# Kernel tuning notes

Measured on AMD Instinct MI355X. Metric: run time of the kernel, lower is better.

Reference implementation:

```python
import jax, jax.numpy as jnp
import numpy as np

B, S = 16, 512
VD, TD, H, NH = 768, 768, 1024, 16
HD = H // NH
MAXREL = 128
THRESH = 2.0 / 3.0


def _bitlinear(x, W, b):
    # BitNet b1.58 eval-mode: ternary-quantize weights, rescale, dense matmul
    s = jnp.clip(jnp.mean(jnp.abs(W)), 1e-5, 1000.0)
    wn = jnp.clip(W / s, -10.0, 10.0)
    q = jnp.where(wn > THRESH, 1.0, jnp.where(wn < -THRESH, -1.0, 0.0))
    return x @ (q * s).T + b


def _ln(x, g, b, eps=1e-5):
    m = jnp.mean(x, axis=-1, keepdims=True)
    v = jnp.mean((x - m) ** 2, axis=-1, keepdims=True)
    return (x - m) * jax.lax.rsqrt(v + eps) * g + b


def setup_inputs() -> dict:
    key = jax.random.key(0)
    ks = jax.random.split(key, 10)
    def n(k, shape, std=0.02):
        return jax.random.normal(k, shape, dtype=jnp.float32) * std
    return dict(
        vision_features=jax.random.normal(ks[0], (B, VD), dtype=jnp.float32),
        text_features=jax.random.normal(ks[1], (B, S, TD), dtype=jnp.float32),
        W_vp=n(ks[2], (H, VD)), b_vp=jnp.zeros((H,), jnp.float32),
        W_tp=n(ks[3], (H, TD)), b_tp=jnp.zeros((H,), jnp.float32),
        W_tqkv=n(ks[4], (3 * H, H)), b_tqkv=jnp.zeros((3 * H,), jnp.float32),
        W_vout=n(ks[5], (H, H)), b_vout=jnp.zeros((H,), jnp.float32),
        W_tout=n(ks[6], (H, H)), b_tout=jnp.zeros((H,), jnp.float32),
        g_tn=jnp.ones((H,), jnp.float32), be_tn=jnp.zeros((H,), jnp.float32),
        g_i2t=jnp.ones((H,), jnp.float32), be_i2t=jnp.zeros((H,), jnp.float32),
        g_t2i=jnp.ones((H,), jnp.float32), be_t2i=jnp.zeros((H,), jnp.float32),
        alpha_i2t=jnp.zeros((1,), jnp.float32),
        alpha_t2i=jnp.zeros((1,), jnp.float32),
        rel_embed=n(ks[7], (2 * MAXREL + 1, NH)),
        text_mask=jnp.ones((B, S), dtype=bool),
    )


def reference(vision_features, text_features, W_vp, b_vp, W_tp, b_tp,
              W_tqkv, b_tqkv, W_vout, b_vout, W_tout, b_tout,
              g_tn, be_tn, g_i2t, be_i2t, g_t2i, be_t2i,
              alpha_i2t, alpha_t2i, rel_embed, text_mask):
    scale = HD ** -0.5
    vision_proj = _bitlinear(vision_features, W_vp, b_vp)            # [B,H]
    text_proj = _bitlinear(text_features, W_tp, b_tp)                # [B,S,H]

    # --- text self-attention with relative-position bias ---
    qkv = _bitlinear(_ln(text_proj, g_tn, be_tn), W_tqkv, b_tqkv)    # [B,S,3H]
    qkv = qkv.reshape(B, S, 3, NH, HD).transpose(2, 0, 3, 1, 4)      # [3,B,nh,S,hd]
    q, k, v = qkv[0], qkv[1], qkv[2]
    attn = jnp.einsum('bhqd,bhkd->bhqk', q, k) * scale
    coords = jnp.arange(S)
    rel = jnp.clip(coords[:, None] - coords[None, :], -MAXREL, MAXREL) + MAXREL
    attn = attn + rel_embed[rel].transpose(2, 0, 1)[None]            # +[1,nh,S,S]
    attn = jnp.where(text_mask[:, None, None, :], attn, -1e9)
    attn = jax.nn.softmax(attn, axis=-1)
    text_self = jnp.einsum('bhqk,bhkd->bhqd', attn, v)
    text_self = text_self.transpose(0, 2, 1, 3).reshape(B, S, H)
    text_self = text_proj + text_self                                # residual

    # --- image -> text cross-attention (vision token queries text) ---
    vq = jnp.broadcast_to(vision_proj[:, None], (B, S, H))
    vq = vq.reshape(B, S, NH, HD).transpose(0, 2, 1, 3)              # [B,nh,S,hd]
    tkv = text_self.reshape(B, S, NH, HD).transpose(0, 2, 1, 3)      # [B,nh,S,hd]
    i2t = jnp.einsum('bhqd,bhkd->bhqk', vq, tkv) * scale
    i2t = jnp.where(text_mask[:, None, None, :], i2t, -1e9)
    i2t = jax.nn.softmax(i2t, axis=-1)
    i2t_out = jnp.einsum('bhqk,bhkd->bhqd', i2t, tkv)
    i2t_out = i2t_out.transpose(0, 2, 1, 3).reshape(B, S, H).mean(axis=1)
    i2t_out = _ln(i2t_out, g_i2t, be_i2t)                            # [B,H]
    fused_vision = vision_proj + alpha_i2t * _bitlinear(i2t_out, W_vout, b_vout)

    # --- text -> image cross-attention (text queries single vision token) ---
    tq = text_self.reshape(B, S, NH, HD).transpose(0, 2, 1, 3)       # [B,nh,S,hd]
    vkv = vision_proj.reshape(B, 1, NH, HD).transpose(0, 2, 1, 3)    # [B,nh,1,hd]
    t2i = jnp.einsum('bhqd,bhkd->bhqk', tq, vkv) * scale             # [B,nh,S,1]
    t2i = jax.nn.softmax(t2i, axis=-1)
    t2i_out = jnp.einsum('bhqk,bhkd->bhqd', t2i, vkv)
    t2i_out = t2i_out.transpose(0, 2, 1, 3).reshape(B, S, H)
    t2i_out = _ln(t2i_out, g_t2i, be_t2i)
    fused_text = text_self + alpha_t2i * _bitlinear(t2i_out, W_tout, b_tout)

    return fused_vision, fused_text
```

## Files before the change

### kernel.cpp

```cpp
#include <hip/hip_runtime.h>
#include <cstdint>

#define B_   16
#define S_   512
#define VD_  768
#define TD_  768
#define H_   1024
#define NH_  16
#define HD_  64
#define H3_  3072

typedef __attribute__((ext_vector_type(8))) short bf16x8;
typedef __attribute__((ext_vector_type(4))) float f32x4;

__device__ __forceinline__ float b2f(unsigned short h) {
  union { unsigned u; float f; } x; x.u = ((unsigned)h) << 16; return x.f;
}
__device__ __forceinline__ unsigned short f2b(float f) {
  union { float f; unsigned u; } x; x.f = f;
  unsigned r = x.u + 0x7fffu + ((x.u >> 16) & 1u);
  return (unsigned short)(r >> 16);
}
__device__ __forceinline__ unsigned cvt_pk_bf16(float lo, float hi) {
  unsigned r;
  __asm__("v_cvt_pk_bf16_f32 %0, %1, %2" : "=v"(r) : "v"(lo), "v"(hi));
  return r;
}
__device__ __forceinline__ float fexp2(float x) {
#if __has_builtin(__builtin_amdgcn_exp2f)
  return __builtin_amdgcn_exp2f(x);
#else
  return exp2f(x);
#endif
}

__device__ __forceinline__ void gload_lds16(const void* g, void* lds) {
  __builtin_amdgcn_global_load_lds(
      (const __attribute__((address_space(1))) unsigned int*)g,
      (__attribute__((address_space(3))) unsigned int*)lds, 16, 0, 0);
}
__device__ __forceinline__ void lds_wave_fence() {
  __asm__ __volatile__("s_waitcnt lgkmcnt(0)" ::: "memory");
}

__global__ __launch_bounds__(256) void k_abssum_cvt(const float* __restrict__ w0, int n0,
                                                    const float* __restrict__ w1, int n1,
                                                    const float* __restrict__ w2, int n2,
                                                    const float* __restrict__ w3, int n3,
                                                    const float* __restrict__ w4, int n4,
                                                    double* __restrict__ partials,
                                                    const float* __restrict__ cvt_in,
                                                    unsigned short* __restrict__ cvt_out,
                                                    int cvt_n4) {
  int y = blockIdx.y;
  if (y == 5) {
    for (int i = blockIdx.x * 256 + threadIdx.x; i < cvt_n4; i += 128 * 256) {
      float4 v = ((const float4*)cvt_in)[i];
      ushort4 o; o.x = f2b(v.x); o.y = f2b(v.y); o.z = f2b(v.z); o.w = f2b(v.w);
      ((ushort4*)cvt_out)[i] = o;
    }
    return;
  }
  const float* w = y == 0 ? w0 : y == 1 ? w1 : y == 2 ? w2 : y == 3 ? w3 : w4;
  int n4q = (y == 0 ? n0 : y == 1 ? n1 : y == 2 ? n2 : y == 3 ? n3 : n4) >> 2;
  double s = 0.0;
  for (int i = blockIdx.x * 256 + threadIdx.x; i < n4q; i += 128 * 256) {
    float4 v = ((const float4*)w)[i];
    s += (double)fabsf(v.x) + (double)fabsf(v.y) + (double)fabsf(v.z) + (double)fabsf(v.w);
  }
#pragma unroll
  for (int off = 32; off > 0; off >>= 1) s += __shfl_down(s, off, 64);
  __shared__ double red[4];
  if ((threadIdx.x & 63) == 0) red[threadIdx.x >> 6] = s;
  __syncthreads();
  if (threadIdx.x == 0)
    partials[y * 128 + blockIdx.x] = red[0] + red[1] + red[2] + red[3];
}

__global__ __launch_bounds__(512) void k_sumfin(const double* __restrict__ partials,
                                                double* __restrict__ sums) {
  int wave = threadIdx.x >> 6, lane = threadIdx.x & 63;
  if (wave >= 5) return;
  double s = partials[wave * 128 + lane] + partials[wave * 128 + 64 + lane];
#pragma unroll
  for (int off = 32; off > 0; off >>= 1) s += __shfl_down(s, off, 64);
  if (lane == 0) sums[wave] = s;
}

__global__ __launch_bounds__(256) void k_quant5(const float* __restrict__ w0, int n0,
                                                const float* __restrict__ w1, int n1,
                                                const float* __restrict__ w2, int n2,
                                                const float* __restrict__ w3, int n3,
                                                const float* __restrict__ w4, int n4,
                                                unsigned short* __restrict__ q0,
                                                unsigned short* __restrict__ q1,
                                                unsigned short* __restrict__ q2,
                                                unsigned short* __restrict__ q3,
                                                unsigned short* __restrict__ q4,
                                                const double* __restrict__ sum,
                                                float* __restrict__ s_out) {
  int y = blockIdx.y;
  const float* w = y == 0 ? w0 : y == 1 ? w1 : y == 2 ? w2 : y == 3 ? w3 : w4;
  unsigned short* q = y == 0 ? q0 : y == 1 ? q1 : y == 2 ? q2 : y == 3 ? q3 : q4;
  int n = y == 0 ? n0 : y == 1 ? n1 : y == 2 ? n2 : y == 3 ? n3 : n4;
  double s = fmin(fmax(sum[y] / (double)n, 1e-5), 1000.0);
  if (blockIdx.x == 0 && threadIdx.x == 0) s_out[y] = (float)s;
  int i = blockIdx.x * 256 + threadIdx.x;
  if (i < n) {
    double wn = (double)w[i] / s;
    unsigned short o = 0;
    if (wn > (2.0 / 3.0)) o = 0x3F80u;
    else if (wn < -(2.0 / 3.0)) o = 0xBF80u;
    q[i] = o;
  }
}

__global__ __launch_bounds__(256) void k_rowmat(const float* __restrict__ A,
                                                const unsigned short* __restrict__ W,
                                                const float* __restrict__ sptr,
                                                const float* __restrict__ bias,
                                                float* __restrict__ Cf,
                                                unsigned short* __restrict__ Cb,
                                                const float* __restrict__ resid,
                                                const float* __restrict__ alpha,
                                                int N, int K) {
  const int t = threadIdx.x, lane = t & 63;
  const int w_idx = blockIdx.x * 4 + (t >> 6);
  const int m = w_idx / N, n = w_idx - m * N;
  const int Kper = K >> 6;
  const float* a = A + (size_t)m * K + lane * Kper;
  const unsigned short* w = W + (size_t)n * K + lane * Kper;
  float acc = 0.f;
  for (int k = 0; k < Kper; k += 4) {
    float4 av = *(const float4*)(a + k);
    ushort4 wv = *(const ushort4*)(w + k);
    acc += av.x * b2f(wv.x) + av.y * b2f(wv.y) + av.z * b2f(wv.z) + av.w * b2f(wv.w);
  }
#pragma unroll
  for (int off = 32; off > 0; off >>= 1) acc += __shfl_down(acc, off, 64);
  if (lane == 0) {
    float v = acc * sptr[0] + bias[n];
    if (resid) v = resid[w_idx] + alpha[0] * v;
    Cf[w_idx] = v;
    if (Cb) Cb[w_idx] = f2b(v);
  }
}

__global__ __launch_bounds__(256) void k_ln(const float* __restrict__ x,
                                            const float* __restrict__ g,
                                            const float* __restrict__ be,
                                            float* __restrict__ of,
                                            unsigned short* __restrict__ ob) {
  int row = blockIdx.x, t = threadIdx.x;
  const float4* xr = (const float4*)(x + (size_t)row * H_);
  float4 v = xr[t];
  float s = v.x + v.y + v.z + v.w;
  float s2 = v.x * v.x + v.y * v.y + v.z * v.z + v.w * v.w;
#pragma unroll
  for (int off = 32; off > 0; off >>= 1) { s += __shfl_down(s, off, 64); s2 += __shfl_down(s2, off, 64); }
  __shared__ float rs[4], rs2[4];
  if ((t & 63) == 0) { rs[t >> 6] = s; rs2[t >> 6] = s2; }
  __syncthreads();
  s = rs[0] + rs[1] + rs[2] + rs[3];
  s2 = rs2[0] + rs2[1] + rs2[2] + rs2[3];
  float mean = s * (1.0f / H_);
  float var = s2 * (1.0f / H_) - mean * mean;
  float rstd = rsqrtf(var + 1e-5f);
  const float4 gv = ((const float4*)g)[t];
  const float4 bv = ((const float4*)be)[t];
  float4 o;
  o.x = (v.x - mean) * rstd * gv.x + bv.x;
  o.y = (v.y - mean) * rstd * gv.y + bv.y;
  o.z = (v.z - mean) * rstd * gv.z + bv.z;
  o.w = (v.w - mean) * rstd * gv.w + bv.w;
  if (of) ((float4*)(of + (size_t)row * H_))[t] = o;
  if (ob) {
    ushort4 ou; ou.x = f2b(o.x); ou.y = f2b(o.y); ou.z = f2b(o.z); ou.w = f2b(o.w);
    ((ushort4*)(ob + (size_t)row * H_))[t] = ou;
  }
}

template <int OUTB, int VT>
__global__ __launch_bounds__(512) void k_gemm(const unsigned short* __restrict__ A,
                                              const unsigned short* __restrict__ W,
                                              const float* __restrict__ sptr,
                                              const float* __restrict__ bias,
                                              float* __restrict__ Cf,
                                              unsigned short* __restrict__ Cb,
                                              unsigned short* __restrict__ vt,
                                              int M, int N, int K) {
  __shared__ __align__(16) unsigned short As[3][128 * 64];
  __shared__ __align__(16) unsigned short Bs[3][256 * 64];
  const int t = threadIdx.x, wave = t >> 6, lane = t & 63, quad = lane >> 4, l16 = lane & 15;
  const int bm = blockIdx.y * 128, bn = blockIdx.x * 256;
  const int wm = (wave >> 2) * 64, wn = (wave & 3) * 64;
  f32x4 acc[4][4];
#pragma unroll
  for (int i = 0; i < 4; ++i)
#pragma unroll
    for (int j = 0; j < 4; ++j) acc[i][j] = f32x4{0.f, 0.f, 0.f, 0.f};

  const int srow = lane >> 3;
  const int kcg = (lane & 7) ^ srow;
  auto stage = [&](int kt, int buf) {
    const int k0 = kt * 64;
#pragma unroll
    for (int c = 0; c < 2; ++c) {
      int row = c * 64 + wave * 8 + srow;
      gload_lds16(A + (size_t)(bm + row) * K + k0 + kcg * 8,
                  &As[buf][(c * 64 + wave * 8) * 64]);
    }
#pragma unroll
    for (int c = 0; c < 4; ++c) {
      int row = c * 64 + wave * 8 + srow;
      gload_lds16(W + (size_t)(bn + row) * K + k0 + kcg * 8,
                  &Bs[buf][(c * 64 + wave * 8) * 64]);
    }
  };

  const int NT = K >> 6;
  stage(0, 0);
  stage(1, 1);
  for (int kt = 0; kt < NT; ++kt) {
    if (kt + 1 < NT) __asm__ __volatile__("s_waitcnt vmcnt(6)" ::: "memory");
    else             __asm__ __volatile__("s_waitcnt vmcnt(0)" ::: "memory");
    __asm__ __volatile__("s_barrier" ::: "memory");
    if (kt + 2 < NT) stage(kt + 2, (kt + 2) % 3);
    const unsigned short* Ab = &As[kt % 3][0];
    const unsigned short* Bb = &Bs[kt % 3][0];
#pragma unroll
    for (int ks = 0; ks < 2; ++ks) {
      bf16x8 af[4], bfr[4];
#pragma unroll
      for (int i = 0; i < 4; ++i) {
        int R = wm + i * 16 + l16;
        af[i] = *(const bf16x8*)&Ab[R * 64 + (((ks * 4 + quad) ^ (R & 7)) * 8)];
      }
#pragma unroll
      for (int j = 0; j < 4; ++j) {
        int R = wn + j * 16 + l16;
        bfr[j] = *(const bf16x8*)&Bb[R * 64 + (((ks * 4 + quad) ^ (R & 7)) * 8)];
      }
      __builtin_amdgcn_s_setprio(1);
#pragma unroll
      for (int i = 0; i < 4; ++i)
#pragma unroll
        for (int j = 0; j < 4; ++j)
          acc[i][j] = __builtin_amdgcn_mfma_f32_16x16x32_bf16(af[i], bfr[j], acc[i][j], 0, 0, 0);
      __builtin_amdgcn_s_setprio(0);
    }
  }
  float s = sptr[0];

  if (VT && bn >= 2 * H_) {
    __syncthreads();
    unsigned short* T = &As[0][0] + wave * 1152;
    const int h = (bn + wn - 2 * H_) >> 6;
    const int b = (bm + wm) >> 9, s0 = (bm + wm) & (S_ - 1);
    const int chunk0 = lane * 2;
#pragma unroll
    for (int j = 0; j < 4; ++j) {
      int n = bn + wn + j * 16 + l16;
      float bv = bias[n];
#pragma unroll
      for (int i = 0; i < 4; ++i)
#pragma unroll
        for (int r = 0; r < 4; ++r)
          T[l16 * 72 + i * 16 + quad * 4 + r] = f2b(acc[i][j][r] * s + bv);
      lds_wave_fence();
#pragma unroll
      for (int cc = 0; cc < 2; ++cc) {
        int ch = chunk0 + cc, dr = ch >> 3, k8 = ch & 7;
        uint4 val = *(const uint4*)&T[dr * 72 + k8 * 8];
        *(uint4*)(vt + ((size_t)(b * NH_ + h) * HD_ + j * 16 + dr) * S_ + s0 + k8 * 8) = val;
      }
      lds_wave_fence();
    }
    return;
  }

#pragma unroll
  for (int j = 0; j < 4; ++j) {
    int n = bn + wn + j * 16 + l16;
    float bv = bias[n];
#pragma unroll
    for (int i = 0; i < 4; ++i) {
#pragma unroll
      for (int r = 0; r < 4; ++r) {
        int m = bm + wm + i * 16 + quad * 4 + r;
        float v = acc[i][j][r] * s + bv;
        if (OUTB) Cb[(size_t)m * N + n] = f2b(v);
        else      Cf[(size_t)m * N + n] = v;
      }
    }
  }
}

__global__ __launch_bounds__(256) void k_flash(const unsigned short* __restrict__ qkv,
                                               const unsigned short* __restrict__ vt,
                                               const float* __restrict__ tp,
                                               const float* __restrict__ rel,
                                               const float* __restrict__ trow,
                                               const float* __restrict__ a_t2i,
                                               float* __restrict__ out_text,
                                               unsigned short* __restrict__ ts_b) {
  const int qt = blockIdx.x, h = blockIdx.y, b = blockIdx.z;
  __shared__ __align__(16) unsigned short Qs[64 * 64];
  __shared__ __align__(16) unsigned short Ks[2][64 * 64];
  __shared__ __align__(16) unsigned short Vs[2][64 * 64];
  __shared__ __align__(16) unsigned short Ps[4][16 * 72];
  __shared__ float rels[257];
  const int t = threadIdx.x, wave = t >> 6, lane = t & 63, quad = lane >> 4, l16 = lane & 15;
  const int srow = lane >> 3;
  const int kcg = (lane & 7) ^ srow;
  const float LOG2E = 1.4426950408889634f;
  const float SC = 0.125f * LOG2E;

  for (int i = t; i < 257; i += 256) rels[i] = rel[i * NH_ + h] * LOG2E;

  auto stage_kv = [&](int kt, int buf) {
#pragma unroll
    for (int c = 0; c < 2; ++c) {
      int row = (wave * 2 + c) * 8 + srow;
      gload_lds16(qkv + (size_t)(b * S_ + kt * 64 + row) * H3_ + H_ + h * HD_ + kcg * 8,
                  &Ks[buf][(wave * 2 + c) * 512]);
      gload_lds16(vt + ((size_t)(b * NH_ + h) * HD_ + row) * S_ + kt * 64 + kcg * 8,
                  &Vs[buf][(wave * 2 + c) * 512]);
    }
  };

#pragma unroll
  for (int c = 0; c < 2; ++c) {
    int row = (wave * 2 + c) * 8 + srow;
    gload_lds16(qkv + (size_t)(b * S_ + qt * 64 + row) * H3_ + h * HD_ + kcg * 8,
                &Qs[(wave * 2 + c) * 512]);
  }
  stage_kv(0, 0);

  float mrun = -1e30f, lrun = 0.f;
  f32x4 o[4];
#pragma unroll
  for (int j = 0; j < 4; ++j) o[j] = f32x4{0.f, 0.f, 0.f, 0.f};

  bf16x8 aq0, aq1;
  bool qloaded = false;
  const int qg = qt * 64 + wave * 16 + l16;

  for (int kt = 0; kt < 8; ++kt) {
    const int cur = kt & 1;
    __syncthreads();
    if (kt < 7) stage_kv(kt + 1, cur ^ 1);

    if (!qloaded) {
      int R = wave * 16 + l16;
      aq0 = *(const bf16x8*)&Qs[R * 64 + ((quad ^ (R & 7)) * 8)];
      aq1 = *(const bf16x8*)&Qs[R * 64 + (((4 + quad) ^ (R & 7)) * 8)];
      qloaded = true;
    }

    const int dq = qt - kt;
    const bool uni = (dq >= 3) || (dq <= -3);
    const float bu = uni ? rels[dq >= 3 ? 256 : 0] : 0.f;

    float pv[4][4];
#pragma unroll
    for (int j = 0; j < 4; ++j) {
      int R = j * 16 + l16;
      bf16x8 kb0 = *(const bf16x8*)&Ks[cur][R * 64 + ((quad ^ (R & 7)) * 8)];
      bf16x8 kb1 = *(const bf16x8*)&Ks[cur][R * 64 + (((4 + quad) ^ (R & 7)) * 8)];
      f32x4 z = f32x4{0.f, 0.f, 0.f, 0.f};
      z = __builtin_amdgcn_mfma_f32_16x16x32_bf16(kb0, aq0, z, 0, 0, 0);
      z = __builtin_amdgcn_mfma_f32_16x16x32_bf16(kb1, aq1, z, 0, 0, 0);
      if (uni) {
#pragma unroll
        for (int r = 0; r < 4; ++r) pv[j][r] = z[r] * SC + bu;
      } else {
        const int kg0 = kt * 64 + j * 16 + quad * 4;
#pragma unroll
        for (int r = 0; r < 4; ++r) {
          int rix = min(max(qg - kg0 - r, -128), 128) + 128;
          pv[j][r] = z[r] * SC + rels[rix];
        }
      }
    }
    float x = pv[0][0];
#pragma unroll
    for (int j = 0; j < 4; ++j)
#pragma unroll
      for (int r = 0; r < 4; ++r) x = fmaxf(x, pv[j][r]);
    x = fmaxf(x, __shfl_xor(x, 16, 64));
    x = fmaxf(x, __shfl_xor(x, 32, 64));
    if (!__all(x <= mrun)) {
      float mn = fmaxf(mrun, x);
      float al = fexp2(mrun - mn);
      mrun = mn;
      lrun *= al;
      float al0 = __shfl(al, quad * 4 + 0, 64);
      float al1 = __shfl(al, quad * 4 + 1, 64);
      float al2 = __shfl(al, quad * 4 + 2, 64);
      float al3 = __shfl(al, quad * 4 + 3, 64);
#pragma unroll
      for (int jd = 0; jd < 4; ++jd) {
        o[jd][0] *= al0; o[jd][1] *= al1; o[jd][2] *= al2; o[jd][3] *= al3;
      }
    }
    float rsum = 0.f;
#pragma unroll
    for (int j = 0; j < 4; ++j)
#pragma unroll
      for (int r = 0; r < 4; ++r) {
        float p = fexp2(pv[j][r] - mrun);
        pv[j][r] = p;
        rsum += p;
      }
    rsum += __shfl_xor(rsum, 16, 64);
    rsum += __shfl_xor(rsum, 32, 64);
    lrun += rsum;
    unsigned char* psb = (unsigned char*)&Ps[wave][0] + l16 * 144 + quad * 8;
#pragma unroll
    for (int j = 0; j < 4; ++j) {
      uint2 pk;
      pk.x = cvt_pk_bf16(pv[j][0], pv[j][1]);
      pk.y = cvt_pk_bf16(pv[j][2], pv[j][3]);
      *(uint2*)(psb + j * 32) = pk;
    }
    lds_wave_fence();
#pragma unroll
    for (int ks = 0; ks < 2; ++ks) {
      bf16x8 ap = *(const bf16x8*)&Ps[wave][l16 * 72 + ks * 32 + quad * 8];
#pragma unroll
      for (int jd = 0; jd < 4; ++jd) {
        int R = jd * 16 + l16;
        int C = ks * 4 + quad;
        bf16x8 vb = *(const bf16x8*)&Vs[cur][R * 64 + ((C ^ (R & 7)) * 8)];
        o[jd] = __builtin_amdgcn_mfma_f32_16x16x32_bf16(ap, vb, o[jd], 0, 0, 0);
      }
    }
  }
  float a2 = a_t2i[0];
  float il[4];
#pragma unroll
  for (int r = 0; r < 4; ++r) {
    float lr = __shfl(lrun, quad * 4 + r, 64);
    il[r] = 1.0f / lr;
  }
#pragma unroll
  for (int jd = 0; jd < 4; ++jd) {
#pragma unroll
    for (int r = 0; r < 4; ++r) {
      int g = b * S_ + qt * 64 + wave * 16 + quad * 4 + r;
      int col = h * HD_ + jd * 16 + l16;
      float ov = o[jd][r] * il[r];
      float ts = tp[(size_t)g * H_ + col] + ov;
      ts_b[(size_t)g * H_ + col] = f2b(ts);
      out_text[(size_t)g * H_ + col] = ts + a2 * trow[b * H_ + col];
    }
  }
}

__global__ __launch_bounds__(256) void k_i2t(const unsigned short* __restrict__ vp_b,
                                             const unsigned short* __restrict__ ts_b,
                                             float* __restrict__ i2t_out) {
  const int h = blockIdx.x & 15, b = blockIdx.x >> 4;
  __shared__ float sc[512];
  __shared__ float red[4];
  __shared__ float qv[64];
  __shared__ float ored[4][64];
  const int t = threadIdx.x;
  if (t < 64) qv[t] = b2f(vp_b[b * H_ + h * HD_ + t]);
  __syncthreads();
  for (int k = t; k < 512; k += 256) {
    const unsigned short* kr = ts_b + (size_t)(b * S_ + k) * H_ + h * HD_;
    float acc = 0.f;
#pragma unroll
    for (int dc = 0; dc < 8; ++dc) {
      uint4 u = *(const uint4*)(kr + dc * 8);
      const unsigned short* p = (const unsigned short*)&u;
#pragma unroll
      for (int i = 0; i < 8; ++i) acc += qv[dc * 8 + i] * b2f(p[i]);
    }
    sc[k] = acc * 0.125f;
  }
  __syncthreads();
  float m = -1e30f;
  for (int k = t; k < 512; k += 256) m = fmaxf(m, sc[k]);
#pragma unroll
  for (int off = 1; off < 64; off <<= 1) m = fmaxf(m, __shfl_xor(m, off, 64));
  if ((t & 63) == 0) red[t >> 6] = m;
  __syncthreads();
  m = fmaxf(fmaxf(red[0], red[1]), fmaxf(red[2], red[3]));
  __syncthreads();
  float ls = 0.f;
  for (int k = t; k < 512; k += 256) { float p = __expf(sc[k] - m); sc[k] = p; ls += p; }
#pragma unroll
  for (int off = 1; off < 64; off <<= 1) ls += __shfl_xor(ls, off, 64);
  if ((t & 63) == 0) red[t >> 6] = ls;
  __syncthreads();
  float tot = red[0] + red[1] + red[2] + red[3];
  const int d = t & 63, grp = t >> 6;
  float acc = 0.f;
  for (int k = grp; k < 512; k += 4)
    acc += sc[k] * b2f(ts_b[(size_t)(b * S_ + k) * H_ + h * HD_ + d]);
  ored[grp][d] = acc;
  __syncthreads();
  if (t < 64)
    i2t_out[b * H_ + h * HD_ + t] = (ored[0][t] + ored[1][t] + ored[2][t] + ored[3][t]) / tot;
}

extern "C" void kernel_launch(void* const* d_in, const int* in_sizes, int n_in,
                              void* d_out, int out_size, void* d_ws, size_t ws_size,
                              hipStream_t stream) {
  const float* vf     = (const float*)d_in[0];
  const float* tf     = (const float*)d_in[1];
  const float* W_vp   = (const float*)d_in[2];
  const float* b_vp   = (const float*)d_in[3];
  const float* W_tp   = (const float*)d_in[4];
  const float* b_tp   = (const float*)d_in[5];
  const float* W_tqkv = (const float*)d_in[6];
  const float* b_tqkv = (const float*)d_in[7];
  const float* W_vout = (const float*)d_in[8];
  const float* b_vout = (const float*)d_in[9];
  const float* W_tout = (const float*)d_in[10];
  const float* b_tout = (const float*)d_in[11];
  const float* g_tn   = (const float*)d_in[12];
  const float* be_tn  = (const float*)d_in[13];
  const float* g_i2t  = (const float*)d_in[14];
  const float* be_i2t = (const float*)d_in[15];
  const float* g_t2i  = (const float*)d_in[16];
  const float* be_t2i = (const float*)d_in[17];
  const float* a_i2t  = (const float*)d_in[18];
  const float* a_t2i  = (const float*)d_in[19];
  const float* rel    = (const float*)d_in[20];

  size_t off = 0;
  auto alloc = [&](size_t bytes) -> void* {
    void* p = (char*)d_ws + off;
    off += (bytes + 255) & ~(size_t)255;
    return p;
  };
  double* sums     = (double*)alloc(64);
  double* partials = (double*)alloc(5 * 128 * 8);
  float* scales    = (float*)alloc(64);
  unsigned short* q_vp   = (unsigned short*)alloc((size_t)H_ * VD_ * 2);
  unsigned short* q_tp   = (unsigned short*)alloc((size_t)H_ * TD_ * 2);
  unsigned short* q_tqkv = (unsigned short*)alloc((size_t)H3_ * H_ * 2);
  unsigned short* q_vout = (unsigned short*)alloc((size_t)H_ * H_ * 2);
  unsigned short* q_tout = (unsigned short*)alloc((size_t)H_ * H_ * 2);
  unsigned short* tf_b   = (unsigned short*)alloc((size_t)B_ * S_ * TD_ * 2);
  float* text_proj       = (float*)alloc((size_t)B_ * S_ * H_ * 4);
  unsigned short* ln_tp  = (unsigned short*)alloc((size_t)B_ * S_ * H_ * 2);
  unsigned short* qkv    = (unsigned short*)alloc((size_t)B_ * S_ * H3_ * 2);
  unsigned short* vt     = (unsigned short*)alloc((size_t)B_ * NH_ * HD_ * S_ * 2);
  unsigned short* ts_b   = (unsigned short*)alloc((size_t)B_ * S_ * H_ * 2);
  float* vision_proj     = (float*)alloc((size_t)B_ * H_ * 4);
  unsigned short* vp_b   = (unsigned short*)alloc((size_t)B_ * H_ * 2);
  float* ln_t2i_f        = (float*)alloc((size_t)B_ * H_ * 4);
  float* trow            = (float*)alloc((size_t)B_ * H_ * 4);
  float* i2t_out         = (float*)alloc((size_t)B_ * H_ * 4);
  float* ln_i2t_f        = (float*)alloc((size_t)B_ * H_ * 4);

  float* out_vision = (float*)d_out;
  float* out_text   = (float*)d_out + B_ * H_;

  k_abssum_cvt<<<dim3(128, 6), 256, 0, stream>>>(W_vp, H_ * VD_, W_tp, H_ * TD_,
                                                 W_tqkv, H3_ * H_, W_vout, H_ * H_,
                                                 W_tout, H_ * H_, partials,
                                                 tf, tf_b, B_ * S_ * TD_ / 4);
  k_sumfin<<<1, 512, 0, stream>>>(partials, sums);
  k_quant5<<<dim3((H3_ * H_ + 255) / 256, 5), 256, 0, stream>>>(
      W_vp, H_ * VD_, W_tp, H_ * TD_, W_tqkv, H3_ * H_, W_vout, H_ * H_, W_tout, H_ * H_,
      q_vp, q_tp, q_tqkv, q_vout, q_tout, sums, scales);

  k_rowmat<<<(B_ * H_) / 4, 256, 0, stream>>>(vf, q_vp, scales + 0, b_vp,
                                              vision_proj, vp_b, nullptr, nullptr, H_, VD_);
  k_ln<<<B_, 256, 0, stream>>>(vision_proj, g_t2i, be_t2i, ln_t2i_f, nullptr);
  k_rowmat<<<(B_ * H_) / 4, 256, 0, stream>>>(ln_t2i_f, q_tout, scales + 4, b_tout,
                                              trow, nullptr, nullptr, nullptr, H_, H_);

  k_gemm<0, 0><<<dim3(H_ / 256, (B_ * S_) / 128), 512, 0, stream>>>(
      tf_b, q_tp, scales + 1, b_tp, text_proj, nullptr, nullptr, B_ * S_, H_, TD_);
  k_ln<<<B_ * S_, 256, 0, stream>>>(text_proj, g_tn, be_tn, nullptr, ln_tp);
  k_gemm<1, 1><<<dim3(H3_ / 256, (B_ * S_) / 128), 512, 0, stream>>>(
      ln_tp, q_tqkv, scales + 2, b_tqkv, nullptr, qkv, vt, B_ * S_, H3_, H_);
  k_flash<<<dim3(S_ / 64, NH_, B_), 256, 0, stream>>>(qkv, vt, text_proj, rel, trow, a_t2i,
                                                      out_text, ts_b);
  k_i2t<<<B_ * NH_, 256, 0, stream>>>(vp_b, ts_b, i2t_out);
  k_ln<<<B_, 256, 0, stream>>>(i2t_out, g_i2t, be_i2t, ln_i2t_f, nullptr);
  k_rowmat<<<(B_ * H_) / 4, 256, 0, stream>>>(ln_i2t_f, q_vout, scales + 3, b_vout,
                                              out_vision, nullptr, vision_proj, a_i2t, H_, H_);
}
```

Measured before the change: 397.0 us.

## Rewrite projection GEMMs as 256-row tiles with ping-pong interleaved prefetch

Replaces the 128x256 triple-buffered GEMM with a 256xNF*64 tile kernel using double-buffered LDS and an 8-wave schedule. Each k-step is split into four quarter phases, with global-to-LDS prefetches spread between barriers and MFMA blocks at raised priority. Tile shapes change to 256x128 for the text projection and 256x192 for the QKV GEMM, giving grids of 8x32 and 16x32 blocks. The goal is better overlap of loads with MFMA and better wave occupancy across CUs. The cost is many more barriers per k-step and a larger per-wave accumulator footprint.

```diff
diff --git a/kernel.cpp b/kernel.cpp
--- a/kernel.cpp
+++ b/kernel.cpp
@@ -180,117 +180,177 @@
   }
 }
 
-template <int OUTB, int VT>
-__global__ __launch_bounds__(512) void k_gemm(const unsigned short* __restrict__ A,
-                                              const unsigned short* __restrict__ W,
-                                              const float* __restrict__ sptr,
-                                              const float* __restrict__ bias,
-                                              float* __restrict__ Cf,
-                                              unsigned short* __restrict__ Cb,
-                                              unsigned short* __restrict__ vt,
-                                              int M, int N, int K) {
-  __shared__ __align__(16) unsigned short As[3][128 * 64];
-  __shared__ __align__(16) unsigned short Bs[3][256 * 64];
-  const int t = threadIdx.x, wave = t >> 6, lane = t & 63, quad = lane >> 4, l16 = lane & 15;
-  const int bm = blockIdx.y * 128, bn = blockIdx.x * 256;
-  const int wm = (wave >> 2) * 64, wn = (wave & 3) * 64;
-  f32x4 acc[4][4];
-#pragma unroll
-  for (int i = 0; i < 4; ++i)
-#pragma unroll
-    for (int j = 0; j < 4; ++j) acc[i][j] = f32x4{0.f, 0.f, 0.f, 0.f};
-
-  const int srow = lane >> 3;
-  const int kcg = (lane & 7) ^ srow;
-  auto stage = [&](int kt, int buf) {
-    const int k0 = kt * 64;
-#pragma unroll
-    for (int c = 0; c < 2; ++c) {
-      int row = c * 64 + wave * 8 + srow;
-      gload_lds16(A + (size_t)(bm + row) * K + k0 + kcg * 8,
-                  &As[buf][(c * 64 + wave * 8) * 64]);
-    }
-#pragma unroll
-    for (int c = 0; c < 4; ++c) {
-      int row = c * 64 + wave * 8 + srow;
-      gload_lds16(W + (size_t)(bn + row) * K + k0 + kcg * 8,
-                  &Bs[buf][(c * 64 + wave * 8) * 64]);
-    }
+template <int NF, int OUTB, int VT>
+__global__ __launch_bounds__(512) void k_gemm8(const unsigned short* __restrict__ A,
+                                               const unsigned short* __restrict__ W,
+                                               const float* __restrict__ sptr,
+                                               const float* __restrict__ bias,
+                                               float* __restrict__ Cf,
+                                               unsigned short* __restrict__ Cb,
+                                               unsigned short* __restrict__ vt,
+                                               int M, int N, int K) {
+  __shared__ __align__(16) unsigned short As[2][256 * 64];
+  __shared__ __align__(16) unsigned short Bs[2][NF * 64 * 64];
+  const int t = threadIdx.x, wave = t >> 6, lane = t & 63;
+  const int quad = lane >> 4, l16 = lane & 15;
+  const int bm = blockIdx.y * 256, bn = blockIdx.x * (NF * 64);
+  const int wg = wave >> 2, wq = wave & 3;
+  const int wn = wq * NF * 16;
+  const int srow = lane >> 3, kc = (lane & 7) ^ srow;
+
+  f32x4 acc[8][NF];
+#pragma unroll
+  for (int i = 0; i < 8; ++i)
+#pragma unroll
+    for (int j = 0; j < NF; ++j) acc[i][j] = f32x4{0.f, 0.f, 0.f, 0.f};
+
+  auto stA = [&](int kt, int r0) {
+    gload_lds16(A + (size_t)(bm + r0 + wave * 8 + srow) * K + kt * 64 + kc * 8,
+                &As[kt & 1][(r0 + wave * 8) * 64]);
   };
+  auto stB = [&](int kt, int r0) {
+    gload_lds16(W + (size_t)(bn + r0 + wave * 8 + srow) * K + kt * 64 + kc * 8,
+                &Bs[kt & 1][(r0 + wave * 8) * 64]);
+  };
 
   const int NT = K >> 6;
-  stage(0, 0);
-  stage(1, 1);
+  stA(0, 0); stA(0, 64); stA(0, 128); stA(0, 192);
+  stB(0, 0); stB(0, 64); if (NF == 3) stB(0, 128);
+  __asm__ __volatile__("s_waitcnt vmcnt(0)" ::: "memory");
+  __builtin_amdgcn_s_barrier();
+
   for (int kt = 0; kt < NT; ++kt) {
-    if (kt + 1 < NT) __asm__ __volatile__("s_waitcnt vmcnt(6)" ::: "memory");
-    else             __asm__ __volatile__("s_waitcnt vmcnt(0)" ::: "memory");
-    __asm__ __volatile__("s_barrier" ::: "memory");
-    if (kt + 2 < NT) stage(kt + 2, (kt + 2) % 3);
-    const unsigned short* Ab = &As[kt % 3][0];
-    const unsigned short* Bb = &Bs[kt % 3][0];
-#pragma unroll
-    for (int ks = 0; ks < 2; ++ks) {
-      bf16x8 af[4], bfr[4];
-#pragma unroll
-      for (int i = 0; i < 4; ++i) {
-        int R = wm + i * 16 + l16;
-        af[i] = *(const bf16x8*)&Ab[R * 64 + (((ks * 4 + quad) ^ (R & 7)) * 8)];
+    const int c = kt & 1;
+    const unsigned short* Ab = &As[c][0];
+    const unsigned short* Bb = &Bs[c][0];
+    const bool pf = (kt + 1 < NT);
+    bf16x8 af[4], bf0[NF], bf1[NF];
+
+#pragma unroll
+    for (int j = 0; j < NF; ++j) {
+      int R = wn + j * 16 + l16;
+      bf0[j] = *(const bf16x8*)&Bb[R * 64 + ((quad ^ (R & 7)) * 8)];
+    }
+#pragma unroll
+    for (int i = 0; i < 4; ++i) {
+      int R = wg * 128 + i * 16 + l16;
+      af[i] = *(const bf16x8*)&Ab[R * 64 + ((quad ^ (R & 7)) * 8)];
+    }
+    if (pf) { stA(kt + 1, 0); stA(kt + 1, 128); }
+    __builtin_amdgcn_s_barrier();
+    __asm__ __volatile__("s_waitcnt lgkmcnt(0)" ::: "memory");
+    __builtin_amdgcn_sched_barrier(0);
+    __builtin_amdgcn_s_setprio(1);
+#pragma unroll
+    for (int i = 0; i < 4; ++i)
+#pragma unroll
+      for (int j = 0; j < NF; ++j)
+        acc[i][j] = __builtin_amdgcn_mfma_f32_16x16x32_bf16(af[i], bf0[j], acc[i][j], 0, 0, 0);
+    __builtin_amdgcn_s_setprio(0);
+    if (pf) __asm__ __volatile__("s_waitcnt vmcnt(2)" ::: "memory");
+    else    __asm__ __volatile__("s_waitcnt vmcnt(0)" ::: "memory");
+    __builtin_amdgcn_s_barrier();
+
+#pragma unroll
+    for (int i = 0; i < 4; ++i) {
+      int R = wg * 128 + 64 + i * 16 + l16;
+      af[i] = *(const bf16x8*)&Ab[R * 64 + ((quad ^ (R & 7)) * 8)];
+    }
+    if (pf) { stB(kt + 1, 0); stB(kt + 1, 64); }
+    __builtin_amdgcn_s_barrier();
+    __asm__ __volatile__("s_waitcnt lgkmcnt(0)" ::: "memory");
+    __builtin_amdgcn_sched_barrier(0);
+    __builtin_amdgcn_s_setprio(1);
+#pragma unroll
+    for (int i = 0; i < 4; ++i)
+#pragma unroll
+      for (int j = 0; j < NF; ++j)
+        acc[4 + i][j] = __builtin_amdgcn_mfma_f32_16x16x32_bf16(af[i], bf0[j], acc[4 + i][j], 0, 0, 0);
+    __builtin_amdgcn_s_setprio(0);
+    __builtin_amdgcn_s_barrier();
+
+#pragma unroll
+    for (int j = 0; j < NF; ++j) {
+      int R = wn + j * 16 + l16;
+      bf1[j] = *(const bf16x8*)&Bb[R * 64 + (((4 + quad) ^ (R & 7)) * 8)];
+    }
+#pragma unroll
+    for (int i = 0; i < 4; ++i) {
+      int R = wg * 128 + i * 16 + l16;
+      af[i] = *(const bf16x8*)&Ab[R * 64 + (((4 + quad) ^ (R & 7)) * 8)];
+    }
+    if (pf && NF == 3) stB(kt + 1, 128);
+    __builtin_amdgcn_s_barrier();
+    __asm__ __volatile__("s_waitcnt lgkmcnt(0)" ::: "memory");
+    __builtin_amdgcn_sched_barrier(0);
+    __builtin_amdgcn_s_setprio(1);
+#pragma unroll
+    for (int i = 0; i < 4; ++i)
+#pragma unroll
+      for (int j = 0; j < NF; ++j)
+        acc[i][j] = __builtin_amdgcn_mfma_f32_16x16x32_bf16(af[i], bf1[j], acc[i][j], 0, 0, 0);
+    __builtin_amdgcn_s_setprio(0);
+    __builtin_amdgcn_s_barrier();
+
+#pragma unroll
+    for (int i = 0; i < 4; ++i) {
+      int R = wg * 128 + 64 + i * 16 + l16;
+      af[i] = *(const bf16x8*)&Ab[R * 64 + (((4 + quad) ^ (R & 7)) * 8)];
+    }
+    if (pf) { stA(kt + 1, 64); stA(kt + 1, 192); }
+    __builtin_amdgcn_s_barrier();
+    __asm__ __volatile__("s_waitcnt lgkmcnt(0)" ::: "memory");
+    __builtin_amdgcn_sched_barrier(0);
+    __builtin_amdgcn_s_setprio(1);
+#pragma unroll
+    for (int i = 0; i < 4; ++i)
+#pragma unroll
+      for (int j = 0; j < NF; ++j)
+        acc[4 + i][j] = __builtin_amdgcn_mfma_f32_16x16x32_bf16(af[i], bf1[j], acc[4 + i][j], 0, 0, 0);
+    __builtin_amdgcn_s_setprio(0);
+    if (pf) __asm__ __volatile__("s_waitcnt vmcnt(2)" ::: "memory");
+    __builtin_amdgcn_s_barrier();
+  }
+  __builtin_amdgcn_sched_barrier(0);
+
+  float s = sptr[0];
+  if (VT) __syncthreads();
+  unsigned short* T = (unsigned short*)&As[0][0] + wave * 1152;
+
+#pragma unroll
+  for (int j = 0; j < NF; ++j) {
+    const int col0 = bn + wn + j * 16;
+    float bv = bias[col0 + l16];
+    if (VT && col0 >= 2 * H_) {
+      const int h = (col0 - 2 * H_) >> 6, d0 = col0 & 63;
+#pragma unroll
+      for (int g = 0; g < 2; ++g) {
+        const int rowbase = bm + wg * 128 + g * 64;
+        const int b = rowbase >> 9, s0v = rowbase & (S_ - 1);
+#pragma unroll
+        for (int i = 0; i < 4; ++i)
+#pragma unroll
+          for (int r = 0; r < 4; ++r)
+            T[l16 * 72 + i * 16 + quad * 4 + r] = f2b(acc[g * 4 + i][j][r] * s + bv);
+        lds_wave_fence();
+#pragma unroll
+        for (int cc = 0; cc < 2; ++cc) {
+          int ch = lane * 2 + cc, dr = ch >> 3, k8 = ch & 7;
+          uint4 val = *(const uint4*)&T[dr * 72 + k8 * 8];
+          *(uint4*)(vt + ((size_t)(b * NH_ + h) * HD_ + d0 + dr) * S_ + s0v + k8 * 8) = val;
+        }
+        lds_wave_fence();
       }
-#pragma unroll
-      for (int j = 0; j < 4; ++j) {
-        int R = wn + j * 16 + l16;
-        bfr[j] = *(const bf16x8*)&Bb[R * 64 + (((ks * 4 + quad) ^ (R & 7)) * 8)];
-      }
-      __builtin_amdgcn_s_setprio(1);
-#pragma unroll
-      for (int i = 0; i < 4; ++i)
-#pragma unroll
-        for (int j = 0; j < 4; ++j)
-          acc[i][j] = __builtin_amdgcn_mfma_f32_16x16x32_bf16(af[i], bfr[j], acc[i][j], 0, 0, 0);
-      __builtin_amdgcn_s_setprio(0);
-    }
-  }
-  float s = sptr[0];
-
-  if (VT && bn >= 2 * H_) {
-    __syncthreads();
-    unsigned short* T = &As[0][0] + wave * 1152;
-    const int h = (bn + wn - 2 * H_) >> 6;
-    const int b = (bm + wm) >> 9, s0 = (bm + wm) & (S_ - 1);
-    const int chunk0 = lane * 2;
-#pragma unroll
-    for (int j = 0; j < 4; ++j) {
-      int n = bn + wn + j * 16 + l16;
-      float bv = bias[n];
-#pragma unroll
-      for (int i = 0; i < 4; ++i)
-#pragma unroll
-        for (int r = 0; r < 4; ++r)
-          T[l16 * 72 + i * 16 + quad * 4 + r] = f2b(acc[i][j][r] * s + bv);
-      lds_wave_fence();
-#pragma unroll
-      for (int cc = 0; cc < 2; ++cc) {
-        int ch = chunk0 + cc, dr = ch >> 3, k8 = ch & 7;
-        uint4 val = *(const uint4*)&T[dr * 72 + k8 * 8];
-        *(uint4*)(vt + ((size_t)(b * NH_ + h) * HD_ + j * 16 + dr) * S_ + s0 + k8 * 8) = val;
-      }
-      lds_wave_fence();
-    }
-    return;
-  }
-
-#pragma unroll
-  for (int j = 0; j < 4; ++j) {
-    int n = bn + wn + j * 16 + l16;
-    float bv = bias[n];
-#pragma unroll
-    for (int i = 0; i < 4; ++i) {
-#pragma unroll
-      for (int r = 0; r < 4; ++r) {
-        int m = bm + wm + i * 16 + quad * 4 + r;
-        float v = acc[i][j][r] * s + bv;
-        if (OUTB) Cb[(size_t)m * N + n] = f2b(v);
-        else      Cf[(size_t)m * N + n] = v;
+    } else {
+#pragma unroll
+      for (int i = 0; i < 8; ++i) {
+#pragma unroll
+        for (int r = 0; r < 4; ++r) {
+          int m = bm + wg * 128 + i * 16 + quad * 4 + r;
+          float v = acc[i][j][r] * s + bv;
+          if (OUTB) Cb[(size_t)m * N + col0 + l16] = f2b(v);
+          else      Cf[(size_t)m * N + col0 + l16] = v;
+        }
       }
     }
   }
@@ -577,10 +637,10 @@
   k_rowmat<<<(B_ * H_) / 4, 256, 0, stream>>>(ln_t2i_f, q_tout, scales + 4, b_tout,
                                               trow, nullptr, nullptr, nullptr, H_, H_);
 
-  k_gemm<0, 0><<<dim3(H_ / 256, (B_ * S_) / 128), 512, 0, stream>>>(
+  k_gemm8<2, 0, 0><<<dim3(H_ / 128, (B_ * S_) / 256), 512, 0, stream>>>(
       tf_b, q_tp, scales + 1, b_tp, text_proj, nullptr, nullptr, B_ * S_, H_, TD_);
   k_ln<<<B_ * S_, 256, 0, stream>>>(text_proj, g_tn, be_tn, nullptr, ln_tp);
-  k_gemm<1, 1><<<dim3(H3_ / 256, (B_ * S_) / 128), 512, 0, stream>>>(
+  k_gemm8<3, 1, 1><<<dim3(H3_ / 192, (B_ * S_) / 256), 512, 0, stream>>>(
       ln_tp, q_tqkv, scales + 2, b_tqkv, nullptr, qkv, vt, B_ * S_, H3_, H_);
   k_flash<<<dim3(S_ / 64, NH_, B_), 256, 0, stream>>>(qkv, vt, text_proj, rel, trow, a_t2i,
                                                       out_text, ts_b);
```

New measurement: 391.1 us. No clear change (-1.5%).
